# Performance work log

Measured on AMD Instinct MI355X. Metric: run time of the kernel, lower is better.

The kernel has to match this reference:

```python
import jax, jax.numpy as jnp
import numpy as np
from jax import lax

B, L, D = 2, 2048, 128
H, HD = 8, 32
WIN = 3

def setup_inputs() -> dict:
    key = jax.random.key(0)
    ks = jax.random.split(key, 7)
    s = 0.05
    return {
        "x":  jax.random.normal(ks[0], (B, L, D), jnp.float32),
        "pe": jax.random.normal(ks[1], (L, D), jnp.float32) * s,
        "Wq": jax.random.normal(ks[2], (D, H * HD), jnp.float32) * s,
        "bq": jnp.zeros((H * HD,), jnp.float32),
        "Wk": jax.random.normal(ks[3], (D, H * HD), jnp.float32) * s,
        "bk": jnp.zeros((H * HD,), jnp.float32),
        "Wv": jax.random.normal(ks[4], (D, H), jnp.float32) * s,
    }

def reference(x, pe, Wq, bq, Wk, bk, Wv):
    b, l, d = x.shape
    h = Wv.shape[1]
    hd = Wq.shape[1] // h
    xp = x + pe                                   # (B,L,D)
    # split heads: Dense output columns [i*hd:(i+1)*hd] -> head i
    q = (xp @ Wq + bq).reshape(b, l, h, hd).transpose(2, 0, 1, 3)  # (H,B,L,hd)
    k = (xp @ Wk + bk).reshape(b, l, h, hd).transpose(2, 0, 1, 3)  # (H,B,L,hd)
    v = jax.nn.sigmoid(x @ Wv).transpose(2, 0, 1)                  # (H,B,L)

    attn = jnp.einsum('hbqd,hbkd->hbqk', q, k) * (float(hd) ** -0.5)
    attn = jax.nn.softmax(attn, axis=-1)          # (H,B,L,L)

    # band_part(0,-1) + diag_part(k=(0,L-1)) (RIGHT_LEFT align) + transpose + reverse(-2,-1)
    # collapses to the skew-gather: R[p, m] = attn[L-1-p-m, L-1-p] for p+m <= L-1 else 0
    p = jnp.arange(l)[:, None]                    # (L,1)
    m = jnp.arange(l)[None, :]                    # (1,L)
    ii = l - 1 - p - m                            # row index  (L,L)
    jj = jnp.broadcast_to(l - 1 - p, (l, l))      # col index  (L,L)
    valid = (ii >= 0)
    R = attn[:, :, jnp.where(valid, ii, 0), jj] * valid.astype(attn.dtype)  # (H,B,L,L)

    R = R * v[:, :, :, None]                      # gate by value, broadcast over distance axis

    # TF avg_pool excludes padding from the divisor
    sums = lax.reduce_window(R, 0.0, lax.add, (1, 1, 1, WIN), (1, 1, 1, 1), 'SAME')
    cnt = lax.reduce_window(jnp.ones((l,), R.dtype), 0.0, lax.add, (WIN,), (1,), 'SAME')
    pooled = sums / cnt                           # (H,B,L,L)

    # global mode: sum over position axis, -> (B, L_dist, H)
    out = pooled.sum(axis=2).transpose(1, 2, 0)
    return out
```

## Files before the change

kernel.cpp:

```cpp
#include <hip/hip_runtime.h>
#include <hip/hip_bf16.h>

#define LSEQ 2048
#define BB 2
#define DD 128
#define HH 8
#define HD 32

#define FPSCALE 524288.0f
#define RFPSCALE (1.0f / 524288.0f)
#define DENSCALE 65536.0f
#define QSCALE 0.25503486f

typedef __bf16 bf8_t __attribute__((ext_vector_type(8)));
typedef float f4_t __attribute__((ext_vector_type(4)));

__global__ __launch_bounds__(256) void k_prep(const float* __restrict__ x,
                                              const float* __restrict__ Wq,
                                              const float* __restrict__ Wk,
                                              const float* __restrict__ Wv,
                                              __bf16* __restrict__ WqT,
                                              __bf16* __restrict__ WkT,
                                              float* __restrict__ w,
                                              int* __restrict__ Si,
                                              int* __restrict__ denI) {
    __shared__ float tile[32][33];
    __shared__ float xs[32 * 132];
    __shared__ float wv[128 * 8];
    int gb = blockIdx.x;
    int tid = threadIdx.x;
    if (gb < 64) {
        int z = gb >> 5, t = gb & 31;
        const float* W = z ? Wk : Wq;
        __bf16* WT = z ? WkT : WqT;
        int d0 = (t & 3) * 32, c0 = (t >> 2) * 32;
        int tr = tid >> 5, tc = tid & 31;
        for (int i = 0; i < 4; i++)
            tile[tr + i * 8][tc] = W[(d0 + tr + i * 8) * 256 + c0 + tc];
        __syncthreads();
        for (int i = 0; i < 4; i++)
            WT[(c0 + tr + i * 8) * 128 + d0 + tc] = (__bf16)tile[tc][tr + i * 8];
    } else if (gb < 192) {
        int r0 = (gb - 64) * 32;
        for (int i = 0; i < 16; i++) {
            int idx = tid + i * 256;
            xs[(idx >> 7) * 132 + (idx & 127)] = x[r0 * 128 + idx];
        }
        for (int i = 0; i < 4; i++) {
            int idx = tid + i * 256;
            wv[idx] = Wv[idx];
        }
        __syncthreads();
        int rl = tid >> 3, h = tid & 7;
        float acc = 0.f;
        #pragma unroll 8
        for (int d = 0; d < 128; d++) acc += xs[rl * 132 + d] * wv[d * 8 + h];
        float sg = 1.f / (1.f + __expf(-acc));
        int r = r0 + rl;
        int b = r >> 11, l = r & (LSEQ - 1);
        w[(h * BB + b) * LSEQ + (LSEQ - 1 - l)] = sg;
    } else if (gb < 320) {
        Si[(gb - 192) * 256 + tid] = 0;
    } else {
        denI[(gb - 320) * 256 + tid] = 0;
    }
}

__global__ __launch_bounds__(256) void k_qk(const float* __restrict__ x,
                                            const float* __restrict__ pe,
                                            const __bf16* __restrict__ WqT,
                                            const __bf16* __restrict__ WkT,
                                            const float* __restrict__ bq,
                                            const float* __restrict__ bk,
                                            __bf16* __restrict__ Qb,
                                            __bf16* __restrict__ Kb) {
    __shared__ __bf16 xs[16][136];
    int tid = threadIdx.x;
    int row0 = blockIdx.x * 16;
    #pragma unroll
    for (int i = 0; i < 8; i++) {
        int idx = tid + i * 256;
        int row = idx >> 7, col = idx & 127;
        xs[row][col] = (__bf16)(x[row0 * 128 + idx] +
                                pe[((row0 + row) & (LSEQ - 1)) * 128 + col]);
    }
    __syncthreads();

    int wid = tid >> 6, lane = tid & 63;
    int col0 = blockIdx.y * 64 + wid * 16;
    bool isK = col0 >= 256;
    int c0 = isK ? col0 - 256 : col0;
    const __bf16* WT = isK ? WkT : WqT;
    const float* bias = isK ? bk : bq;
    __bf16* Out = isK ? Kb : Qb;

    int lm = lane & 15, lq = lane >> 4;
    f4_t acc = {0.f, 0.f, 0.f, 0.f};
    const __bf16* bptr = WT + (c0 + lm) * 128 + lq * 8;
    #pragma unroll
    for (int s = 0; s < 4; s++) {
        bf8_t a = *(const bf8_t*)(&xs[lm][lq * 8 + s * 32]);
        bf8_t bfr = *(const bf8_t*)(bptr + s * 32);
        acc = __builtin_amdgcn_mfma_f32_16x16x32_bf16(a, bfr, acc, 0, 0, 0);
    }
    int c = c0 + lm;
    float bv = bias[c];
    float qs = isK ? 1.f : QSCALE;
    int h = c >> 5, hd = c & 31;
    #pragma unroll
    for (int r = 0; r < 4; r++) {
        int row = row0 + lq * 4 + r;
        int b_ = row >> 11, l = row & (LSEQ - 1);
        Out[((h * BB + b_) * LSEQ + l) * HD + hd] = (__bf16)((acc[r] + bv) * qs);
    }
}

__global__ __launch_bounds__(256) void k_den(const __bf16* __restrict__ Qb,
                                             const __bf16* __restrict__ Kb,
                                             int* __restrict__ denI) {
    int hb = blockIdx.z;
    int q0 = blockIdx.y * 64;
    int kbase = blockIdx.x * 512;
    int wid = threadIdx.x >> 6, lane = threadIdx.x & 63;
    int lm = lane & 15, lq = lane >> 4;
    int qw0 = q0 + wid * 16;

    bf8_t aq = *(const bf8_t*)(Qb + (hb * LSEQ + qw0 + lm) * HD + lq * 8);
    const __bf16* Khb = Kb + hb * LSEQ * HD;

    float dsum[4] = {0.f, 0.f, 0.f, 0.f};
    #pragma unroll 4
    for (int s = 0; s < 32; s++) {
        bf8_t bk_ = *(const bf8_t*)(Khb + (kbase + s * 16 + lm) * HD + lq * 8);
        f4_t z = {0.f, 0.f, 0.f, 0.f};
        f4_t sc = __builtin_amdgcn_mfma_f32_16x16x32_bf16(aq, bk_, z, 0, 0, 0);
        #pragma unroll
        for (int r = 0; r < 4; r++) dsum[r] += exp2f(sc[r]);
    }
    #pragma unroll
    for (int r = 0; r < 4; r++) {
        float v = dsum[r];
        v += __shfl_xor(v, 1);
        v += __shfl_xor(v, 2);
        v += __shfl_xor(v, 4);
        v += __shfl_xor(v, 8);
        dsum[r] = v;
    }
    if (lm == 0) {
        #pragma unroll
        for (int r = 0; r < 4; r++)
            atomicAdd(&denI[hb * LSEQ + qw0 + lq * 4 + r],
                      __float2int_rn(dsum[r] * DENSCALE));
    }
}

__global__ __launch_bounds__(256) void k_scat(const __bf16* __restrict__ Qb,
                                              const __bf16* __restrict__ Kb,
                                              const float* __restrict__ w,
                                              const int* __restrict__ denI,
                                              int* __restrict__ S) {
    int hb = blockIdx.z;
    int q0 = blockIdx.y * 64;
    int kc0 = blockIdx.x * 256;
    if (kc0 + 256 <= q0) return;

    __shared__ int Sloc[4 * 320];
    __shared__ float wt[256];
    int tid = threadIdx.x;
    for (int i = tid; i < 1280; i += 256) Sloc[i] = 0;
    wt[tid] = w[hb * LSEQ + kc0 + tid] * FPSCALE;

    int wid = tid >> 6, lane = tid & 63;
    int lm = lane & 15, lq = lane >> 4;
    int qw0 = q0 + wid * 16;
    bf8_t aq = *(const bf8_t*)(Qb + (hb * LSEQ + qw0 + lm) * HD + lq * 8);
    float rdv[4];
    #pragma unroll
    for (int r = 0; r < 4; r++)
        rdv[r] = DENSCALE / (float)denI[hb * LSEQ + qw0 + lq * 4 + r];
    __syncthreads();

    const __bf16* Khb = Kb + hb * LSEQ * HD;
    int mbase = kc0 - q0 - 63;
    int qrow = qw0 + lq * 4;
    int* mySloc = Sloc + wid * 320;

    #pragma unroll 4
    for (int sub = 0; sub < 16; sub++) {
        int k0s = kc0 + sub * 16;
        if (k0s + 15 < qw0) continue;
        bf8_t bk_ = *(const bf8_t*)(Khb + (k0s + lm) * HD + lq * 8);
        f4_t z = {0.f, 0.f, 0.f, 0.f};
        f4_t sc = __builtin_amdgcn_mfma_f32_16x16x32_bf16(aq, bk_, z, 0, 0, 0);
        float wvs = wt[sub * 16 + lm];
        int kcol = k0s + lm;
        #pragma unroll
        for (int r = 0; r < 4; r++) {
            int m = kcol - (qrow + r);
            if (m >= 0) {
                int iv = __float2int_rn(exp2f(sc[r]) * rdv[r] * wvs);
                atomicAdd(&mySloc[m - mbase], iv);
            }
        }
    }
    __syncthreads();
    for (int i = tid; i < 320; i += 256) {
        int m = mbase + i;
        int v = Sloc[i] + Sloc[320 + i] + Sloc[640 + i] + Sloc[960 + i];
        if (m >= 0 && m < LSEQ && v != 0)
            atomicAdd(&S[hb * LSEQ + m], v);
    }
}

__global__ __launch_bounds__(256) void k_out(const int* __restrict__ S,
                                             float* __restrict__ out) {
    int idx = blockIdx.x * 256 + threadIdx.x;
    int h = idx & 7;
    int m = (idx >> 3) & (LSEQ - 1);
    int b = idx >> 14;
    const int* Sr = S + (h * BB + b) * LSEQ;
    float s = (float)Sr[m];
    float cnt = 3.f;
    if (m > 0) s += (float)Sr[m - 1]; else cnt = 2.f;
    if (m < LSEQ - 1) s += (float)Sr[m + 1]; else cnt = 2.f;
    out[idx] = s * RFPSCALE / cnt;
}

extern "C" void kernel_launch(void* const* d_in, const int* in_sizes, int n_in,
                              void* d_out, int out_size, void* d_ws, size_t ws_size,
                              hipStream_t stream) {
    const float* x  = (const float*)d_in[0];
    const float* pe = (const float*)d_in[1];
    const float* Wq = (const float*)d_in[2];
    const float* bq = (const float*)d_in[3];
    const float* Wk = (const float*)d_in[4];
    const float* bk = (const float*)d_in[5];
    const float* Wv = (const float*)d_in[6];
    float* out = (float*)d_out;

    char* ws = (char*)d_ws;
    int*    Si   = (int*)(ws);
    float*  w    = (float*)(ws + 131072);
    __bf16* Qb   = (__bf16*)(ws + 262144);
    __bf16* Kb   = (__bf16*)(ws + 262144 + 2097152);
    int*    denI = (int*)(ws + 262144 + 4194304);
    __bf16* WqT  = (__bf16*)(ws + 262144 + 4194304 + 131072);
    __bf16* WkT  = (__bf16*)(ws + 262144 + 4194304 + 131072 + 65536);

    k_prep<<<448, 256, 0, stream>>>(x, Wq, Wk, Wv, WqT, WkT, w, Si, denI);
    k_qk<<<dim3(256, 8), 256, 0, stream>>>(x, pe, WqT, WkT, bq, bk, Qb, Kb);
    k_den<<<dim3(4, 32, 16), 256, 0, stream>>>(Qb, Kb, denI);
    k_scat<<<dim3(8, 32, 16), 256, 0, stream>>>(Qb, Kb, w, denI, Si);
    k_out<<<128, 256, 0, stream>>>(Si, out);
}
```

Baseline: 133.3 us.

## Fuse kernels into three launches with in-block softmax denominator and full-row scatter

Merges weight transpose into the QK projection kernel (each block transposes its Wq/Wk slice into shared memory), and fuses the denominator pass with the scatter pass so each block computes the full row sum itself before scattering into a 2048-wide shared accumulator per wave. This removes two kernel launches, the denI atomic buffer and its zeroing, and the global re-read of denominators. In exchange each k_B block serially loops over all keys twice with only 512 blocks, so parallelism is much lower and per-block work is unbalanced (early q rows do far more), and shared memory use rises to 40KB per block.

Result: slower. 154.6 us (+15.9%).

```diff
diff --git a/kernel.cpp b/kernel.cpp
--- a/kernel.cpp
+++ b/kernel.cpp
@@ -9,119 +9,111 @@
 
 #define FPSCALE 524288.0f
 #define RFPSCALE (1.0f / 524288.0f)
-#define DENSCALE 65536.0f
 #define QSCALE 0.25503486f
 
 typedef __bf16 bf8_t __attribute__((ext_vector_type(8)));
 typedef float f4_t __attribute__((ext_vector_type(4)));
 
-__global__ __launch_bounds__(256) void k_prep(const float* __restrict__ x,
-                                              const float* __restrict__ Wq,
-                                              const float* __restrict__ Wk,
-                                              const float* __restrict__ Wv,
-                                              __bf16* __restrict__ WqT,
-                                              __bf16* __restrict__ WkT,
-                                              float* __restrict__ w,
-                                              int* __restrict__ Si,
-                                              int* __restrict__ denI) {
-    __shared__ float tile[32][33];
-    __shared__ float xs[32 * 132];
-    __shared__ float wv[128 * 8];
+__global__ __launch_bounds__(256) void k_A(const float* __restrict__ x,
+                                           const float* __restrict__ pe,
+                                           const float* __restrict__ Wq,
+                                           const float* __restrict__ Wk,
+                                           const float* __restrict__ Wv,
+                                           const float* __restrict__ bq,
+                                           const float* __restrict__ bk,
+                                           float* __restrict__ w,
+                                           __bf16* __restrict__ Qb,
+                                           __bf16* __restrict__ Kb,
+                                           int* __restrict__ Si) {
+    __shared__ __align__(16) char smem[21760];
     int gb = blockIdx.x;
     int tid = threadIdx.x;
-    if (gb < 64) {
-        int z = gb >> 5, t = gb & 31;
-        const float* W = z ? Wk : Wq;
-        __bf16* WT = z ? WkT : WqT;
-        int d0 = (t & 3) * 32, c0 = (t >> 2) * 32;
-        int tr = tid >> 5, tc = tid & 31;
-        for (int i = 0; i < 4; i++)
-            tile[tr + i * 8][tc] = W[(d0 + tr + i * 8) * 256 + c0 + tc];
+
+    if (gb < 2048) {
+        __bf16 (*Wt)[136] = (__bf16(*)[136])smem;
+        __bf16 (*xs)[136] = (__bf16(*)[136])(smem + 64 * 136 * 2);
+        int rb = gb & 255, y = gb >> 8;
+        int row0 = rb * 16;
+        bool isK = y >= 4;
+        int cbase = (isK ? y - 4 : y) * 64;
+        const float* W = isK ? Wk : Wq;
+
+        #pragma unroll
+        for (int i = 0; i < 8; i++) {
+            int idx = tid + i * 256;
+            int row = idx >> 7, col = idx & 127;
+            xs[row][col] = (__bf16)(x[row0 * 128 + idx] +
+                                    pe[((row0 + row) & (LSEQ - 1)) * 128 + col]);
+        }
+        #pragma unroll
+        for (int i = 0; i < 32; i++) {
+            int idx = tid + i * 256;
+            int d = idx >> 6, c = idx & 63;
+            Wt[c][d] = (__bf16)(W[d * 256 + cbase + c]);
+        }
         __syncthreads();
-        for (int i = 0; i < 4; i++)
-            WT[(c0 + tr + i * 8) * 128 + d0 + tc] = (__bf16)tile[tc][tr + i * 8];
-    } else if (gb < 192) {
-        int r0 = (gb - 64) * 32;
+
+        int wid = tid >> 6, lane = tid & 63;
+        int lm = lane & 15, lq = lane >> 4;
+        int c0loc = wid * 16;
+        f4_t acc = {0.f, 0.f, 0.f, 0.f};
+        #pragma unroll
+        for (int s = 0; s < 4; s++) {
+            bf8_t a = *(const bf8_t*)(&xs[lm][lq * 8 + s * 32]);
+            bf8_t bfr = *(const bf8_t*)(&Wt[c0loc + lm][lq * 8 + s * 32]);
+            acc = __builtin_amdgcn_mfma_f32_16x16x32_bf16(a, bfr, acc, 0, 0, 0);
+        }
+        int c = cbase + c0loc + lm;
+        float bv = (isK ? bk : bq)[c];
+        float qs = isK ? 1.f : QSCALE;
+        __bf16* Out = isK ? Kb : Qb;
+        int h = c >> 5, hd = c & 31;
+        #pragma unroll
+        for (int r = 0; r < 4; r++) {
+            int row = row0 + lq * 4 + r;
+            int b_ = row >> 11, l = row & (LSEQ - 1);
+            Out[((h * BB + b_) * LSEQ + l) * HD + hd] = (__bf16)((acc[r] + bv) * qs);
+        }
+    } else if (gb < 2176) {
+        float* xsf = (float*)smem;
+        float* wvf = (float*)(smem + 32 * 132 * 4);
+        int r0 = (gb - 2048) * 32;
         for (int i = 0; i < 16; i++) {
             int idx = tid + i * 256;
-            xs[(idx >> 7) * 132 + (idx & 127)] = x[r0 * 128 + idx];
+            xsf[(idx >> 7) * 132 + (idx & 127)] = x[r0 * 128 + idx];
         }
         for (int i = 0; i < 4; i++) {
             int idx = tid + i * 256;
-            wv[idx] = Wv[idx];
+            wvf[idx] = Wv[idx];
         }
         __syncthreads();
         int rl = tid >> 3, h = tid & 7;
         float acc = 0.f;
         #pragma unroll 8
-        for (int d = 0; d < 128; d++) acc += xs[rl * 132 + d] * wv[d * 8 + h];
+        for (int d = 0; d < 128; d++) acc += xsf[rl * 132 + d] * wvf[d * 8 + h];
         float sg = 1.f / (1.f + __expf(-acc));
         int r = r0 + rl;
         int b = r >> 11, l = r & (LSEQ - 1);
         w[(h * BB + b) * LSEQ + (LSEQ - 1 - l)] = sg;
-    } else if (gb < 320) {
-        Si[(gb - 192) * 256 + tid] = 0;
     } else {
-        denI[(gb - 320) * 256 + tid] = 0;
-    }
-}
-
-__global__ __launch_bounds__(256) void k_qk(const float* __restrict__ x,
-                                            const float* __restrict__ pe,
-                                            const __bf16* __restrict__ WqT,
-                                            const __bf16* __restrict__ WkT,
-                                            const float* __restrict__ bq,
-                                            const float* __restrict__ bk,
-                                            __bf16* __restrict__ Qb,
-                                            __bf16* __restrict__ Kb) {
-    __shared__ __bf16 xs[16][136];
+        Si[(gb - 2176) * 256 + tid] = 0;
+    }
+}
+
+__global__ __launch_bounds__(256) void k_B(const __bf16* __restrict__ Qb,
+                                           const __bf16* __restrict__ Kb,
+                                           const float* __restrict__ w,
+                                           int* __restrict__ Si) {
+    int hb = blockIdx.y;
+    int q0 = blockIdx.x * 64;
     int tid = threadIdx.x;
-    int row0 = blockIdx.x * 16;
-    #pragma unroll
-    for (int i = 0; i < 8; i++) {
-        int idx = tid + i * 256;
-        int row = idx >> 7, col = idx & 127;
-        xs[row][col] = (__bf16)(x[row0 * 128 + idx] +
-                                pe[((row0 + row) & (LSEQ - 1)) * 128 + col]);
-    }
-    __syncthreads();
+
+    __shared__ int Sloc[4 * 2048];
+    __shared__ float wt[2048];
+    for (int i = tid; i < 8192; i += 256) Sloc[i] = 0;
+    for (int i = tid; i < 2048; i += 256) wt[i] = w[hb * LSEQ + i];
 
     int wid = tid >> 6, lane = tid & 63;
-    int col0 = blockIdx.y * 64 + wid * 16;
-    bool isK = col0 >= 256;
-    int c0 = isK ? col0 - 256 : col0;
-    const __bf16* WT = isK ? WkT : WqT;
-    const float* bias = isK ? bk : bq;
-    __bf16* Out = isK ? Kb : Qb;
-
-    int lm = lane & 15, lq = lane >> 4;
-    f4_t acc = {0.f, 0.f, 0.f, 0.f};
-    const __bf16* bptr = WT + (c0 + lm) * 128 + lq * 8;
-    #pragma unroll
-    for (int s = 0; s < 4; s++) {
-        bf8_t a = *(const bf8_t*)(&xs[lm][lq * 8 + s * 32]);
-        bf8_t bfr = *(const bf8_t*)(bptr + s * 32);
-        acc = __builtin_amdgcn_mfma_f32_16x16x32_bf16(a, bfr, acc, 0, 0, 0);
-    }
-    int c = c0 + lm;
-    float bv = bias[c];
-    float qs = isK ? 1.f : QSCALE;
-    int h = c >> 5, hd = c & 31;
-    #pragma unroll
-    for (int r = 0; r < 4; r++) {
-        int row = row0 + lq * 4 + r;
-        int b_ = row >> 11, l = row & (LSEQ - 1);
-        Out[((h * BB + b_) * LSEQ + l) * HD + hd] = (__bf16)((acc[r] + bv) * qs);
-    }
-}
-
-__global__ __launch_bounds__(256) void k_den(const __bf16* __restrict__ Qb,
-                                             const __bf16* __restrict__ Kb,
-                                             int* __restrict__ denI) {
-    int hb = blockIdx.z;
-    int q0 = blockIdx.y * 64;
-    int kbase = blockIdx.x * 512;
-    int wid = threadIdx.x >> 6, lane = threadIdx.x & 63;
     int lm = lane & 15, lq = lane >> 4;
     int qw0 = q0 + wid * 16;
 
@@ -130,13 +122,14 @@
 
     float dsum[4] = {0.f, 0.f, 0.f, 0.f};
     #pragma unroll 4
-    for (int s = 0; s < 32; s++) {
-        bf8_t bk_ = *(const bf8_t*)(Khb + (kbase + s * 16 + lm) * HD + lq * 8);
+    for (int s = 0; s < 128; s++) {
+        bf8_t bk_ = *(const bf8_t*)(Khb + (s * 16 + lm) * HD + lq * 8);
         f4_t z = {0.f, 0.f, 0.f, 0.f};
         f4_t sc = __builtin_amdgcn_mfma_f32_16x16x32_bf16(aq, bk_, z, 0, 0, 0);
         #pragma unroll
         for (int r = 0; r < 4; r++) dsum[r] += exp2f(sc[r]);
     }
+    float rdv[4];
     #pragma unroll
     for (int r = 0; r < 4; r++) {
         float v = dsum[r];
@@ -144,71 +137,33 @@
         v += __shfl_xor(v, 2);
         v += __shfl_xor(v, 4);
         v += __shfl_xor(v, 8);
-        dsum[r] = v;
-    }
-    if (lm == 0) {
-        #pragma unroll
-        for (int r = 0; r < 4; r++)
-            atomicAdd(&denI[hb * LSEQ + qw0 + lq * 4 + r],
-                      __float2int_rn(dsum[r] * DENSCALE));
-    }
-}
-
-__global__ __launch_bounds__(256) void k_scat(const __bf16* __restrict__ Qb,
-                                              const __bf16* __restrict__ Kb,
-                                              const float* __restrict__ w,
-                                              const int* __restrict__ denI,
-                                              int* __restrict__ S) {
-    int hb = blockIdx.z;
-    int q0 = blockIdx.y * 64;
-    int kc0 = blockIdx.x * 256;
-    if (kc0 + 256 <= q0) return;
-
-    __shared__ int Sloc[4 * 320];
-    __shared__ float wt[256];
-    int tid = threadIdx.x;
-    for (int i = tid; i < 1280; i += 256) Sloc[i] = 0;
-    wt[tid] = w[hb * LSEQ + kc0 + tid] * FPSCALE;
-
-    int wid = tid >> 6, lane = tid & 63;
-    int lm = lane & 15, lq = lane >> 4;
-    int qw0 = q0 + wid * 16;
-    bf8_t aq = *(const bf8_t*)(Qb + (hb * LSEQ + qw0 + lm) * HD + lq * 8);
-    float rdv[4];
-    #pragma unroll
-    for (int r = 0; r < 4; r++)
-        rdv[r] = DENSCALE / (float)denI[hb * LSEQ + qw0 + lq * 4 + r];
+        rdv[r] = FPSCALE / v;
+    }
     __syncthreads();
 
-    const __bf16* Khb = Kb + hb * LSEQ * HD;
-    int mbase = kc0 - q0 - 63;
+    int* mySloc = Sloc + wid * 2048;
     int qrow = qw0 + lq * 4;
-    int* mySloc = Sloc + wid * 320;
-
-    #pragma unroll 4
-    for (int sub = 0; sub < 16; sub++) {
-        int k0s = kc0 + sub * 16;
-        if (k0s + 15 < qw0) continue;
+    for (int k0s = qw0; k0s < LSEQ; k0s += 16) {
         bf8_t bk_ = *(const bf8_t*)(Khb + (k0s + lm) * HD + lq * 8);
         f4_t z = {0.f, 0.f, 0.f, 0.f};
         f4_t sc = __builtin_amdgcn_mfma_f32_16x16x32_bf16(aq, bk_, z, 0, 0, 0);
-        float wvs = wt[sub * 16 + lm];
         int kcol = k0s + lm;
+        float wvs = wt[kcol];
         #pragma unroll
         for (int r = 0; r < 4; r++) {
             int m = kcol - (qrow + r);
             if (m >= 0) {
                 int iv = __float2int_rn(exp2f(sc[r]) * rdv[r] * wvs);
-                atomicAdd(&mySloc[m - mbase], iv);
+                atomicAdd(&mySloc[m], iv);
             }
         }
     }
     __syncthreads();
-    for (int i = tid; i < 320; i += 256) {
-        int m = mbase + i;
-        int v = Sloc[i] + Sloc[320 + i] + Sloc[640 + i] + Sloc[960 + i];
-        if (m >= 0 && m < LSEQ && v != 0)
-            atomicAdd(&S[hb * LSEQ + m], v);
+    int mlen = LSEQ - q0;
+    for (int i = tid; i < mlen; i += 256) {
+        int v = Sloc[i] + Sloc[2048 + i] + Sloc[4096 + i] + Sloc[6144 + i];
+        if (v != 0)
+            atomicAdd(&Si[hb * LSEQ + i], v);
     }
 }
 
@@ -243,13 +198,8 @@
     float*  w    = (float*)(ws + 131072);
     __bf16* Qb   = (__bf16*)(ws + 262144);
     __bf16* Kb   = (__bf16*)(ws + 262144 + 2097152);
-    int*    denI = (int*)(ws + 262144 + 4194304);
-    __bf16* WqT  = (__bf16*)(ws + 262144 + 4194304 + 131072);
-    __bf16* WkT  = (__bf16*)(ws + 262144 + 4194304 + 131072 + 65536);
-
-    k_prep<<<448, 256, 0, stream>>>(x, Wq, Wk, Wv, WqT, WkT, w, Si, denI);
-    k_qk<<<dim3(256, 8), 256, 0, stream>>>(x, pe, WqT, WkT, bq, bk, Qb, Kb);
-    k_den<<<dim3(4, 32, 16), 256, 0, stream>>>(Qb, Kb, denI);
-    k_scat<<<dim3(8, 32, 16), 256, 0, stream>>>(Qb, Kb, w, denI, Si);
+
+    k_A<<<2304, 256, 0, stream>>>(x, pe, Wq, Wk, Wv, bq, bk, w, Qb, Kb, Si);
+    k_B<<<dim3(32, 16), 256, 0, stream>>>(Qb, Kb, w, Si);
     k_out<<<128, 256, 0, stream>>>(Si, out);
 }
```

## Fuse weight transpose, Q/K projection and zeroing into one prep kernel; peel diagonal tile

Applied to the files above, without the earlier changes.

Merges k_prep and k_qk into a single kernel k_A. Each projection block stages a 64-row x+pe tile and transposes its 64-column slice of Wq/Wk into shared memory, then issues four MFMAs per weight fragment. This removes a launch and the global WqT/WkT round trip, and vectorises the zeroing with int4 stores. In k_scat, the loop over k sub-tiles now starts at the first relevant tile and peels it, so the remaining tiles skip both the per-iteration skip test and the m>=0 check. In exchange, each projection block recomputes the weight transpose, and every row block redoes the same weight work.

Result: faster. 128.1 us, median of 2 (-3.9%).

```diff
diff --git a/kernel.cpp b/kernel.cpp
--- a/kernel.cpp
+++ b/kernel.cpp
@@ -13,105 +13,115 @@
 #define QSCALE 0.25503486f
 
 typedef __bf16 bf8_t __attribute__((ext_vector_type(8)));
+typedef __bf16 bf4_t __attribute__((ext_vector_type(4)));
 typedef float f4_t __attribute__((ext_vector_type(4)));
 
-__global__ __launch_bounds__(256) void k_prep(const float* __restrict__ x,
-                                              const float* __restrict__ Wq,
-                                              const float* __restrict__ Wk,
-                                              const float* __restrict__ Wv,
-                                              __bf16* __restrict__ WqT,
-                                              __bf16* __restrict__ WkT,
-                                              float* __restrict__ w,
-                                              int* __restrict__ Si,
-                                              int* __restrict__ denI) {
-    __shared__ float tile[32][33];
-    __shared__ float xs[32 * 132];
-    __shared__ float wv[128 * 8];
+__global__ __launch_bounds__(256) void k_A(const float* __restrict__ x,
+                                           const float* __restrict__ pe,
+                                           const float* __restrict__ Wq,
+                                           const float* __restrict__ Wk,
+                                           const float* __restrict__ Wv,
+                                           const float* __restrict__ bq,
+                                           const float* __restrict__ bk,
+                                           float* __restrict__ w,
+                                           __bf16* __restrict__ Qb,
+                                           __bf16* __restrict__ Kb,
+                                           int* __restrict__ Si,
+                                           int* __restrict__ denI) {
+    __shared__ __align__(16) char smem[34816];
     int gb = blockIdx.x;
     int tid = threadIdx.x;
-    if (gb < 64) {
-        int z = gb >> 5, t = gb & 31;
-        const float* W = z ? Wk : Wq;
-        __bf16* WT = z ? WkT : WqT;
-        int d0 = (t & 3) * 32, c0 = (t >> 2) * 32;
-        int tr = tid >> 5, tc = tid & 31;
-        for (int i = 0; i < 4; i++)
-            tile[tr + i * 8][tc] = W[(d0 + tr + i * 8) * 256 + c0 + tc];
+
+    if (gb < 512) {
+        __bf16* xs = (__bf16*)smem;
+        __bf16* Wt = (__bf16*)(smem + 64 * 136 * 2);
+        int jr = gb >> 3, y = gb & 7;
+        int row0 = jr * 64;
+        bool isK = y >= 4;
+        int cbase = (y & 3) * 64;
+        const float* W = isK ? Wk : Wq;
+
+        #pragma unroll
+        for (int i = 0; i < 8; i++) {
+            int idx4 = tid + i * 256;
+            int row = idx4 >> 5, col4 = idx4 & 31;
+            float4 xv = ((const float4*)x)[row0 * 32 + idx4];
+            float4 pv = ((const float4*)pe)[((row0 + row) & (LSEQ - 1)) * 32 + col4];
+            bf4_t o = {(__bf16)(xv.x + pv.x), (__bf16)(xv.y + pv.y),
+                       (__bf16)(xv.z + pv.z), (__bf16)(xv.w + pv.w)};
+            *(bf4_t*)&xs[row * 136 + col4 * 4] = o;
+        }
+        #pragma unroll
+        for (int i = 0; i < 8; i++) {
+            int idx4 = tid + i * 256;
+            int d = idx4 >> 4, c4 = (idx4 & 15) * 4;
+            float4 wv4 = *(const float4*)(W + d * 256 + cbase + c4);
+            Wt[(c4 + 0) * 136 + d] = (__bf16)wv4.x;
+            Wt[(c4 + 1) * 136 + d] = (__bf16)wv4.y;
+            Wt[(c4 + 2) * 136 + d] = (__bf16)wv4.z;
+            Wt[(c4 + 3) * 136 + d] = (__bf16)wv4.w;
+        }
         __syncthreads();
-        for (int i = 0; i < 4; i++)
-            WT[(c0 + tr + i * 8) * 128 + d0 + tc] = (__bf16)tile[tc][tr + i * 8];
-    } else if (gb < 192) {
-        int r0 = (gb - 64) * 32;
+
+        int wid = tid >> 6, lane = tid & 63;
+        int lm = lane & 15, lq = lane >> 4;
+        int c0loc = wid * 16;
+        f4_t acc0 = {0,0,0,0}, acc1 = {0,0,0,0}, acc2 = {0,0,0,0}, acc3 = {0,0,0,0};
+        #pragma unroll
+        for (int s = 0; s < 4; s++) {
+            bf8_t bw = *(const bf8_t*)&Wt[(c0loc + lm) * 136 + lq * 8 + s * 32];
+            bf8_t a0 = *(const bf8_t*)&xs[(0  + lm) * 136 + lq * 8 + s * 32];
+            bf8_t a1 = *(const bf8_t*)&xs[(16 + lm) * 136 + lq * 8 + s * 32];
+            bf8_t a2 = *(const bf8_t*)&xs[(32 + lm) * 136 + lq * 8 + s * 32];
+            bf8_t a3 = *(const bf8_t*)&xs[(48 + lm) * 136 + lq * 8 + s * 32];
+            acc0 = __builtin_amdgcn_mfma_f32_16x16x32_bf16(a0, bw, acc0, 0, 0, 0);
+            acc1 = __builtin_amdgcn_mfma_f32_16x16x32_bf16(a1, bw, acc1, 0, 0, 0);
+            acc2 = __builtin_amdgcn_mfma_f32_16x16x32_bf16(a2, bw, acc2, 0, 0, 0);
+            acc3 = __builtin_amdgcn_mfma_f32_16x16x32_bf16(a3, bw, acc3, 0, 0, 0);
+        }
+        int c = cbase + c0loc + lm;
+        float bv = (isK ? bk : bq)[c];
+        float qs = isK ? 1.f : QSCALE;
+        __bf16* Out = isK ? Kb : Qb;
+        int h = c >> 5, hd = c & 31;
+        f4_t accs[4] = {acc0, acc1, acc2, acc3};
+        #pragma unroll
+        for (int rs = 0; rs < 4; rs++) {
+            #pragma unroll
+            for (int r = 0; r < 4; r++) {
+                int row = row0 + rs * 16 + lq * 4 + r;
+                int b_ = row >> 11, l = row & (LSEQ - 1);
+                Out[((h * BB + b_) * LSEQ + l) * HD + hd] =
+                    (__bf16)((accs[rs][r] + bv) * qs);
+            }
+        }
+    } else if (gb < 640) {
+        float* xsf = (float*)smem;
+        float* wvf = (float*)(smem + 32 * 132 * 4);
+        int r0 = (gb - 512) * 32;
         for (int i = 0; i < 16; i++) {
             int idx = tid + i * 256;
-            xs[(idx >> 7) * 132 + (idx & 127)] = x[r0 * 128 + idx];
+            xsf[(idx >> 7) * 132 + (idx & 127)] = x[r0 * 128 + idx];
         }
         for (int i = 0; i < 4; i++) {
             int idx = tid + i * 256;
-            wv[idx] = Wv[idx];
+            wvf[idx] = Wv[idx];
         }
         __syncthreads();
         int rl = tid >> 3, h = tid & 7;
         float acc = 0.f;
         #pragma unroll 8
-        for (int d = 0; d < 128; d++) acc += xs[rl * 132 + d] * wv[d * 8 + h];
+        for (int d = 0; d < 128; d++) acc += xsf[rl * 132 + d] * wvf[d * 8 + h];
         float sg = 1.f / (1.f + __expf(-acc));
         int r = r0 + rl;
         int b = r >> 11, l = r & (LSEQ - 1);
         w[(h * BB + b) * LSEQ + (LSEQ - 1 - l)] = sg;
-    } else if (gb < 320) {
-        Si[(gb - 192) * 256 + tid] = 0;
+    } else if (gb < 672) {
+        int4 z = {0, 0, 0, 0};
+        ((int4*)Si)[(gb - 640) * 256 + tid] = z;
     } else {
-        denI[(gb - 320) * 256 + tid] = 0;
-    }
-}
-
-__global__ __launch_bounds__(256) void k_qk(const float* __restrict__ x,
-                                            const float* __restrict__ pe,
-                                            const __bf16* __restrict__ WqT,
-                                            const __bf16* __restrict__ WkT,
-                                            const float* __restrict__ bq,
-                                            const float* __restrict__ bk,
-                                            __bf16* __restrict__ Qb,
-                                            __bf16* __restrict__ Kb) {
-    __shared__ __bf16 xs[16][136];
-    int tid = threadIdx.x;
-    int row0 = blockIdx.x * 16;
-    #pragma unroll
-    for (int i = 0; i < 8; i++) {
-        int idx = tid + i * 256;
-        int row = idx >> 7, col = idx & 127;
-        xs[row][col] = (__bf16)(x[row0 * 128 + idx] +
-                                pe[((row0 + row) & (LSEQ - 1)) * 128 + col]);
-    }
-    __syncthreads();
-
-    int wid = tid >> 6, lane = tid & 63;
-    int col0 = blockIdx.y * 64 + wid * 16;
-    bool isK = col0 >= 256;
-    int c0 = isK ? col0 - 256 : col0;
-    const __bf16* WT = isK ? WkT : WqT;
-    const float* bias = isK ? bk : bq;
-    __bf16* Out = isK ? Kb : Qb;
-
-    int lm = lane & 15, lq = lane >> 4;
-    f4_t acc = {0.f, 0.f, 0.f, 0.f};
-    const __bf16* bptr = WT + (c0 + lm) * 128 + lq * 8;
-    #pragma unroll
-    for (int s = 0; s < 4; s++) {
-        bf8_t a = *(const bf8_t*)(&xs[lm][lq * 8 + s * 32]);
-        bf8_t bfr = *(const bf8_t*)(bptr + s * 32);
-        acc = __builtin_amdgcn_mfma_f32_16x16x32_bf16(a, bfr, acc, 0, 0, 0);
-    }
-    int c = c0 + lm;
-    float bv = bias[c];
-    float qs = isK ? 1.f : QSCALE;
-    int h = c >> 5, hd = c & 31;
-    #pragma unroll
-    for (int r = 0; r < 4; r++) {
-        int row = row0 + lq * 4 + r;
-        int b_ = row >> 11, l = row & (LSEQ - 1);
-        Out[((h * BB + b_) * LSEQ + l) * HD + hd] = (__bf16)((acc[r] + bv) * qs);
+        int4 z = {0, 0, 0, 0};
+        ((int4*)denI)[(gb - 672) * 256 + tid] = z;
     }
 }
 
@@ -185,14 +195,14 @@
     int qrow = qw0 + lq * 4;
     int* mySloc = Sloc + wid * 320;
 
-    #pragma unroll 4
-    for (int sub = 0; sub < 16; sub++) {
-        int k0s = kc0 + sub * 16;
-        if (k0s + 15 < qw0) continue;
+    int sub_start = (qw0 > kc0) ? ((qw0 - kc0) >> 4) : 0;
+
+    {
+        int k0s = kc0 + sub_start * 16;
         bf8_t bk_ = *(const bf8_t*)(Khb + (k0s + lm) * HD + lq * 8);
         f4_t z = {0.f, 0.f, 0.f, 0.f};
         f4_t sc = __builtin_amdgcn_mfma_f32_16x16x32_bf16(aq, bk_, z, 0, 0, 0);
-        float wvs = wt[sub * 16 + lm];
+        float wvs = wt[sub_start * 16 + lm];
         int kcol = k0s + lm;
         #pragma unroll
         for (int r = 0; r < 4; r++) {
@@ -201,6 +211,21 @@
                 int iv = __float2int_rn(exp2f(sc[r]) * rdv[r] * wvs);
                 atomicAdd(&mySloc[m - mbase], iv);
             }
+        }
+    }
+    #pragma unroll 4
+    for (int sub = sub_start + 1; sub < 16; sub++) {
+        int k0s = kc0 + sub * 16;
+        bf8_t bk_ = *(const bf8_t*)(Khb + (k0s + lm) * HD + lq * 8);
+        f4_t z = {0.f, 0.f, 0.f, 0.f};
+        f4_t sc = __builtin_amdgcn_mfma_f32_16x16x32_bf16(aq, bk_, z, 0, 0, 0);
+        float wvs = wt[sub * 16 + lm];
+        int kcol = k0s + lm;
+        #pragma unroll
+        for (int r = 0; r < 4; r++) {
+            int m = kcol - (qrow + r);
+            int iv = __float2int_rn(exp2f(sc[r]) * rdv[r] * wvs);
+            atomicAdd(&mySloc[m - mbase], iv);
         }
     }
     __syncthreads();
@@ -244,11 +269,8 @@
     __bf16* Qb   = (__bf16*)(ws + 262144);
     __bf16* Kb   = (__bf16*)(ws + 262144 + 2097152);
     int*    denI = (int*)(ws + 262144 + 4194304);
-    __bf16* WqT  = (__bf16*)(ws + 262144 + 4194304 + 131072);
-    __bf16* WkT  = (__bf16*)(ws + 262144 + 4194304 + 131072 + 65536);
-
-    k_prep<<<448, 256, 0, stream>>>(x, Wq, Wk, Wv, WqT, WkT, w, Si, denI);
-    k_qk<<<dim3(256, 8), 256, 0, stream>>>(x, pe, WqT, WkT, bq, bk, Qb, Kb);
+
+    k_A<<<704, 256, 0, stream>>>(x, pe, Wq, Wk, Wv, bq, bk, w, Qb, Kb, Si, denI);
     k_den<<<dim3(4, 32, 16), 256, 0, stream>>>(Qb, Kb, denI);
     k_scat<<<dim3(8, 32, 16), 256, 0, stream>>>(Qb, Kb, w, denI, Si);
     k_out<<<128, 256, 0, stream>>>(Si, out);
```
